# Optimization experiments

Hardware: AMD Instinct MI355X
Metric: run time of the kernel (lower is better)

## Reference

```python
import jax, jax.numpy as jnp
import numpy as np

N_NODES = 51200
N_GRAPHS = 64
NODES_PER_GRAPH = 800
N_EDGES = 819200
DIM_IN = 128
DIM_HIDDEN = 64
HEADS = 3
DIM_OUT = 64


def leaky(x, slope):
    return jnp.where(x >= 0, x, slope * x)


def setup_inputs() -> dict:
    key = jax.random.key(0)
    ks = jax.random.split(key, 12)
    s = lambda fan_in: 1.0 / np.sqrt(fan_in)
    X = jax.random.normal(ks[0], (N_NODES, DIM_IN), dtype=jnp.float32)
    edge_indices = jax.random.randint(ks[1], (2, N_EDGES), 0, N_NODES, dtype=jnp.int32)
    ptr = (jnp.arange(N_GRAPHS + 1, dtype=jnp.int32) * NODES_PER_GRAPH)
    # linearSeq: Linear(dim_in, dim_hidden) + LeakyReLU
    W1 = jax.random.uniform(ks[2], (DIM_IN, DIM_HIDDEN), jnp.float32, -s(DIM_IN), s(DIM_IN))
    b1 = jax.random.uniform(ks[3], (DIM_HIDDEN,), jnp.float32, -s(DIM_IN), s(DIM_IN))
    # GATConv params: lin_src/lin_dst (no bias), att_src/att_dst, bias (concat=False -> out_channels)
    W_src = jax.random.uniform(ks[4], (DIM_HIDDEN, HEADS * DIM_HIDDEN), jnp.float32, -s(DIM_HIDDEN), s(DIM_HIDDEN))
    W_dst = jax.random.uniform(ks[5], (DIM_HIDDEN, HEADS * DIM_HIDDEN), jnp.float32, -s(DIM_HIDDEN), s(DIM_HIDDEN))
    att_src = jax.random.normal(ks[6], (HEADS, DIM_HIDDEN), dtype=jnp.float32) * 0.1
    att_dst = jax.random.normal(ks[7], (HEADS, DIM_HIDDEN), dtype=jnp.float32) * 0.1
    gat_bias = jnp.zeros((DIM_HIDDEN,), dtype=jnp.float32)
    # linear_final: Linear(2*dim_hidden, dim_out)
    Wf = jax.random.uniform(ks[8], (2 * DIM_HIDDEN, DIM_OUT), jnp.float32, -s(2 * DIM_HIDDEN), s(2 * DIM_HIDDEN))
    bf = jax.random.uniform(ks[9], (DIM_OUT,), jnp.float32, -s(2 * DIM_HIDDEN), s(2 * DIM_HIDDEN))
    return {"X": X, "W1": W1, "b1": b1, "W_src": W_src, "W_dst": W_dst,
            "att_src": att_src, "att_dst": att_dst, "gat_bias": gat_bias,
            "Wf": Wf, "bf": bf, "edge_indices": edge_indices, "ptr": ptr}


def reference(X, W1, b1, W_src, W_dst, att_src, att_dst, gat_bias, Wf, bf, edge_indices, ptr):
    N = X.shape[0]
    src, dst = edge_indices[0], edge_indices[1]  # message flows src -> dst
    # input projection
    h = leaky(X @ W1 + b1, 0.01)                                  # [N, DH]
    # GATConv (heads=3, concat=False, add_self_loops=False)
    x_src = (h @ W_src).reshape(N, HEADS, DIM_HIDDEN)             # [N, H, C]
    x_dst = (h @ W_dst).reshape(N, HEADS, DIM_HIDDEN)
    a_src = jnp.einsum('nhc,hc->nh', x_src, att_src)              # [N, H]
    a_dst = jnp.einsum('nhc,hc->nh', x_dst, att_dst)
    logits = leaky(a_src[src] + a_dst[dst], 0.2)                  # [E, H]
    # segment softmax over incoming edges of each target node
    m = jax.ops.segment_max(logits, dst, num_segments=N)          # [N, H]
    e = jnp.exp(logits - m[dst])
    denom = jax.ops.segment_sum(e, dst, num_segments=N)           # [N, H]
    attn = e / denom[dst]                                         # [E, H]
    msg = x_src[src] * attn[..., None]                            # [E, H, C]
    agg = jax.ops.segment_sum(msg, dst, num_segments=N)           # [N, H, C]
    out = agg.mean(axis=1) + gat_bias                             # concat=False -> head mean
    # final head
    cat = jnp.concatenate([h, out], axis=1)                       # [N, 2*DH]
    y = leaky(cat, 0.01) @ Wf + bf                                # [N, DO]
    # aggregate_using_ptr: mean-pool nodes per graph using CSR ptr
    node_graph = jnp.searchsorted(ptr, jnp.arange(N), side='right') - 1
    sums = jax.ops.segment_sum(y, node_graph, num_segments=ptr.shape[0] - 1)
    counts = (ptr[1:] - ptr[:-1]).astype(y.dtype)
    pooled = sums / counts[:, None]                               # [n_graphs, DO]
    return pooled, attn
```

## Files before the change

kernel.cpp:

```cpp
#include <hip/hip_runtime.h>
#include <hip/hip_bf16.h>

#define N_NODES   51200
#define N_GRAPHS  64
#define N_EDGES   819200
#define DIM_IN    128
#define DH        64
#define HEADS     3
#define DIM_OUT   64
#define CAP       96
#define NPART     512
#define PART_SZ   100
#define PBUF_CAP  2048
#define BIN_BLOCKS  400
#define PREP_BLOCKS 116
#define SC_BLOCKS   NPART
#define K1_BLOCKS   (N_NODES / 64)

typedef __hip_bfloat16 bf16;
typedef short bf16x8 __attribute__((ext_vector_type(8)));
typedef float f32x4  __attribute__((ext_vector_type(4)));

__device__ __forceinline__ float b2f(bf16 x) { return __bfloat162float(x); }
__device__ __forceinline__ bf16  f2b(float x) { return __float2bfloat16(x); }
__device__ __forceinline__ short f2bs(float x) { return (short)__bfloat16_as_ushort(f2b(x)); }
__device__ __forceinline__ float leaky(float x, float s) { return x >= 0.f ? x : s * x; }
__device__ __forceinline__ float ldin(const void* p, size_t i, int f32) {
    return f32 ? ((const float*)p)[i] : b2f(((const bf16*)p)[i]);
}
__device__ __forceinline__ bf16x8 ld8(const void* p, size_t i, int f32) {
    if (!f32) return *((const bf16x8*)((const short*)p + i));
    const float* f = (const float*)p + i;
    bf16x8 r;
    #pragma unroll
    for (int j = 0; j < 8; ++j) r[j] = f2bs(f[j]);
    return r;
}

__global__ __launch_bounds__(256) void k_bin_prep(const int* __restrict__ src,
                                                  const int* __restrict__ dst,
                                                  int* __restrict__ pcur,
                                                  unsigned* __restrict__ pbuf,
                                                  const void* __restrict__ X,
                                                  const void* __restrict__ W1,
                                                  const void* __restrict__ Wsrc,
                                                  const void* __restrict__ Wdst,
                                                  const void* __restrict__ Wf,
                                                  const void* __restrict__ att_src,
                                                  const void* __restrict__ att_dst,
                                                  int* __restrict__ flag,
                                                  short* __restrict__ W1t,
                                                  short* __restrict__ Wspt,
                                                  short* __restrict__ Wft,
                                                  short* __restrict__ Wat) {
    const int tid = threadIdx.x;
    if (blockIdx.x < BIN_BLOCKS) {
        __shared__ int cnt[NPART];
        __shared__ int base[NPART];
        cnt[tid] = 0; cnt[tid + 256] = 0;
        __syncthreads();
        const int e0 = blockIdx.x * 2048;
        unsigned pk[8]; int pp[8]; int rr[8];
        #pragma unroll
        for (int t = 0; t < 8; ++t) {
            int e = e0 + t * 256 + tid;
            int s = src[e], d = dst[e];
            int p = d / PART_SZ;
            pk[t] = ((unsigned)s << 16) | (unsigned)(d - p * PART_SZ);
            pp[t] = p;
            rr[t] = atomicAdd(&cnt[p], 1);
        }
        __syncthreads();
        base[tid]       = atomicAdd(&pcur[tid],       cnt[tid]);
        base[tid + 256] = atomicAdd(&pcur[tid + 256], cnt[tid + 256]);
        __syncthreads();
        #pragma unroll
        for (int t = 0; t < 8; ++t) {
            int o = base[pp[t]] + rr[t];
            if (o < PBUF_CAP) pbuf[(size_t)pp[t] * PBUF_CAP + o] = pk[t];
        }
        return;
    }
    if (blockIdx.x < BIN_BLOCKS + PREP_BLOCKS) {
        unsigned ex = (((const unsigned short*)X)[2 * tid] >> 7) & 0xFF;
        int c = __syncthreads_count(ex >= 110 && ex <= 135);
        const int f32 = (c < 128) ? 1 : 0;
        int idx = (blockIdx.x - BIN_BLOCKS) * 256 + tid;
        if (idx < 8192) {
            int n = idx >> 7, k = idx & 127;
            W1t[idx] = f2bs(ldin(W1, (size_t)k * 64 + n, f32));
        } else if (idx < 20480) {
            int j = idx - 8192;
            int col = j / 192;
            int rem = j - col * 192;
            int hh = rem >> 6, kk = rem & 63;
            Wspt[j] = f2bs(ldin(Wsrc, (size_t)kk * 192 + hh * 64 + col, f32) * (1.0f / 3.0f));
        } else if (idx < 28672) {
            int j = idx - 20480;
            int n = j >> 7, k = j & 127;
            Wft[j] = f2bs(ldin(Wf, (size_t)k * 64 + n, f32));
        } else if (idx < 29696) {
            int j = idx - 28672;
            int n = j >> 6, k = j & 63;
            float v = 0.f;
            if (n < 3) {
                for (int c2 = 0; c2 < 64; ++c2)
                    v += ldin(Wsrc, (size_t)k * 192 + n * 64 + c2, f32) * ldin(att_src, n * 64 + c2, f32);
            } else if (n < 6) {
                for (int c2 = 0; c2 < 64; ++c2)
                    v += ldin(Wdst, (size_t)k * 192 + (n - 3) * 64 + c2, f32) * ldin(att_dst, (n - 3) * 64 + c2, f32);
            }
            Wat[j] = f2bs(v);
        }
        return;
    }
    __shared__ int cntp;
    if (tid == 0) cntp = 0;
    __syncthreads();
    int local = 0;
    const unsigned short* Xu = (const unsigned short*)X;
    for (int i = tid * 2; i < 8192; i += 512) {
        unsigned e = (Xu[i] >> 7) & 0xFF;
        if (e >= 110 && e <= 135) local++;
    }
    atomicAdd(&cntp, local);
    __syncthreads();
    if (tid == 0) *flag = (cntp < 2048) ? 1 : 0;
}

__global__ __launch_bounds__(256) void k_scatter_k1(const unsigned* __restrict__ pbuf,
                                                    const int* __restrict__ pcur,
                                                    int* __restrict__ cursor,
                                                    unsigned short* __restrict__ bucket,
                                                    const void* __restrict__ X,
                                                    const short* __restrict__ W1t,
                                                    const short* __restrict__ Wat,
                                                    const void* __restrict__ b1,
                                                    const int* __restrict__ flagp,
                                                    bf16* __restrict__ h_bf,
                                                    unsigned char* __restrict__ h8,
                                                    float* __restrict__ a_src4,
                                                    float* __restrict__ a_dst4) {
    __shared__ short hs[64 * 72];
    __shared__ int cnt2[PART_SZ];
    const int tid = threadIdx.x;
    if (blockIdx.x < SC_BLOCKS) {
        const int p = blockIdx.x;
        const int nbase = p * PART_SZ;
        for (int i = tid; i < PART_SZ; i += 256) cnt2[i] = 0;
        __syncthreads();
        const int pc = min(pcur[p], PBUF_CAP);
        const unsigned* pb = pbuf + (size_t)p * PBUF_CAP;
        for (int i = tid; i < pc; i += 256) {
            unsigned pk = pb[i];
            int dl = (int)(pk & 0xFFFFu);
            int pos = atomicAdd(&cnt2[dl], 1);
            if (pos < CAP) bucket[(size_t)(nbase + dl) * CAP + pos] = (unsigned short)(pk >> 16);
        }
        __syncthreads();
        for (int i = tid; i < PART_SZ; i += 256) cursor[nbase + i] = cnt2[i];
        return;
    }
    const int f32 = *flagp;
    const int w    = tid >> 6;
    const int lane = tid & 63;
    const int lm   = lane & 15;
    const int q    = lane >> 4;
    const int row0 = (blockIdx.x - SC_BLOCKS) * 64;

    const float bias = ldin(b1, w * 16 + lm, f32);
    for (int mt = 0; mt < 4; ++mt) {
        f32x4 acc = {0.f, 0.f, 0.f, 0.f};
        #pragma unroll
        for (int kc = 0; kc < 4; ++kc) {
            bf16x8 a = ld8(X, (size_t)(row0 + mt * 16 + lm) * 128 + kc * 32 + q * 8, f32);
            bf16x8 b = *((const bf16x8*)(W1t + (size_t)(w * 16 + lm) * 128 + kc * 32 + q * 8));
            acc = __builtin_amdgcn_mfma_f32_16x16x32_bf16(a, b, acc, 0, 0, 0);
        }
        #pragma unroll
        for (int r = 0; r < 4; ++r) {
            int row = mt * 16 + q * 4 + r;
            float v = leaky(acc[r] + bias, 0.01f);
            short hv = f2bs(v);
            hs[row * 72 + w * 16 + lm] = hv;
            h_bf[(size_t)(row0 + row) * 64 + w * 16 + lm] = __ushort_as_bfloat16((unsigned short)hv);
            h8[(size_t)(row0 + row) * 64 + w * 16 + lm] =
                (unsigned char)__builtin_amdgcn_cvt_pk_fp8_f32(v, 0.f, 0, false);
        }
    }
    __syncthreads();
    {
        const int mt = w;
        bf16x8 a0  = *((const bf16x8*)(hs + (mt * 16 + lm) * 72 + q * 8));
        bf16x8 a1  = *((const bf16x8*)(hs + (mt * 16 + lm) * 72 + 32 + q * 8));
        bf16x8 b0  = *((const bf16x8*)(Wat + (size_t)lm * 64 + q * 8));
        bf16x8 b1v = *((const bf16x8*)(Wat + (size_t)lm * 64 + 32 + q * 8));
        f32x4 acca = {0.f, 0.f, 0.f, 0.f};
        acca = __builtin_amdgcn_mfma_f32_16x16x32_bf16(a0, b0, acca, 0, 0, 0);
        acca = __builtin_amdgcn_mfma_f32_16x16x32_bf16(a1, b1v, acca, 0, 0, 0);
        if (lm < 6) {
            #pragma unroll
            for (int r = 0; r < 4; ++r) {
                int row = row0 + mt * 16 + q * 4 + r;
                if (lm < 3) a_src4[(size_t)row * 4 + lm] = acca[r];
                else        a_dst4[(size_t)row * 4 + (lm - 3)] = acca[r];
            }
        }
    }
}

__global__ __launch_bounds__(256) void edge_kernel(const unsigned short* __restrict__ bucket,
                                                   const int* __restrict__ cursor,
                                                   const float* __restrict__ a_src4,
                                                   const float* __restrict__ a_dst4,
                                                   const unsigned char* __restrict__ h8,
                                                   float4* __restrict__ dstinfo,
                                                   bf16* __restrict__ wagg) {
    const int lane = threadIdx.x & 63;
    const int w = threadIdx.x >> 6;
    const int n = blockIdx.x * 4 + w;
    const int dg = min(cursor[n], CAP);
    const float4 ad = ((const float4*)a_dst4)[n];
    __shared__ float4 buf[4][64];
    float den0 = 0.f, den1 = 0.f, den2 = 0.f;
    float acc0 = 0.f, acc1 = 0.f, acc2 = 0.f;
    for (int c0 = 0; c0 < dg; c0 += 64) {
        int cnt = min(64, dg - c0);
        if (lane < cnt) {
            int s = bucket[(size_t)n * CAP + c0 + lane];
            const float4 as = ((const float4*)a_src4)[s];
            float e0 = __expf(leaky(as.x + ad.x, 0.2f));
            float e1 = __expf(leaky(as.y + ad.y, 0.2f));
            float e2 = __expf(leaky(as.z + ad.z, 0.2f));
            den0 += e0; den1 += e1; den2 += e2;
            buf[w][lane] = make_float4(e0, e1, e2, __int_as_float(s));
        }
        asm volatile("s_waitcnt lgkmcnt(0)" ::: "memory");
        int j = 0;
        for (; j + 8 <= cnt; j += 8) {
            float4 r[8]; int hv[8];
            #pragma unroll
            for (int u = 0; u < 8; ++u) r[u] = buf[w][j + u];
            #pragma unroll
            for (int u = 0; u < 8; ++u)
                hv[u] = (int)h8[(((unsigned)__float_as_int(r[u].w)) << 6) | (unsigned)lane];
            #pragma unroll
            for (int u = 0; u < 8; ++u) {
                float f = __builtin_amdgcn_cvt_f32_fp8(hv[u], 0);
                acc0 += r[u].x * f; acc1 += r[u].y * f; acc2 += r[u].z * f;
            }
        }
        for (; j < cnt; ++j) {
            float4 r = buf[w][j];
            int hvv = (int)h8[(((unsigned)__float_as_int(r.w)) << 6) | (unsigned)lane];
            float f = __builtin_amdgcn_cvt_f32_fp8(hvv, 0);
            acc0 += r.x * f; acc1 += r.y * f; acc2 += r.z * f;
        }
    }
    #pragma unroll
    for (int off = 32; off >= 1; off >>= 1) {
        den0 += __shfl_xor(den0, off);
        den1 += __shfl_xor(den1, off);
        den2 += __shfl_xor(den2, off);
    }
    float inv0 = den0 > 0.f ? 1.f / den0 : 0.f;
    float inv1 = den1 > 0.f ? 1.f / den1 : 0.f;
    float inv2 = den2 > 0.f ? 1.f / den2 : 0.f;
    size_t wb = (size_t)n * 192;
    wagg[wb + lane]       = f2b(acc0 * inv0);
    wagg[wb + 64 + lane]  = f2b(acc1 * inv1);
    wagg[wb + 128 + lane] = f2b(acc2 * inv2);
    if (lane == 0) {
        dstinfo[(size_t)n * 2 + 0] = make_float4(ad.x, ad.y, ad.z, 0.f);
        dstinfo[(size_t)n * 2 + 1] = make_float4(inv0, inv1, inv2, 0.f);
    }
}

__global__ __launch_bounds__(256) void attn_g3_kernel(const int* __restrict__ src,
                                                      const int* __restrict__ dst,
                                                      const float* __restrict__ a_src4,
                                                      const float4* __restrict__ dstinfo,
                                                      const bf16* __restrict__ h_bf,
                                                      const bf16* __restrict__ wagg,
                                                      const short* __restrict__ Wspt,
                                                      const short* __restrict__ Wft,
                                                      const void* __restrict__ gat_bias,
                                                      const void* __restrict__ bfv,
                                                      const int* __restrict__ flagp,
                                                      const int* __restrict__ gptr,
                                                      float* __restrict__ psum,
                                                      int* __restrict__ done,
                                                      void* __restrict__ d_out) {
    const int f32 = *flagp;
    __shared__ short cs[64 * 136];
    __shared__ int sptr[N_GRAPHS + 1];
    __shared__ int rowg_s[64];
    __shared__ int readyg[64];
    __shared__ int nready;
    if (blockIdx.x < N_EDGES / 256) {
        int e = blockIdx.x * 256 + threadIdx.x;
        int s = src[e], d = dst[e];
        const float4 as = ((const float4*)a_src4)[s];
        const float4 ad = dstinfo[(size_t)d * 2 + 0];
        const float4 cv = dstinfo[(size_t)d * 2 + 1];
        float a0 = __expf(leaky(as.x + ad.x, 0.2f)) * cv.x;
        float a1 = __expf(leaky(as.y + ad.y, 0.2f)) * cv.y;
        float a2 = __expf(leaky(as.z + ad.z, 0.2f)) * cv.z;
        size_t o = (size_t)N_GRAPHS * DIM_OUT + (size_t)e * 3;
        if (f32) {
            float* p = (float*)d_out;
            p[o] = a0; p[o + 1] = a1; p[o + 2] = a2;
        } else {
            bf16* p = (bf16*)d_out;
            p[o] = f2b(a0); p[o + 1] = f2b(a1); p[o + 2] = f2b(a2);
        }
        return;
    }
    const int bid  = blockIdx.x - N_EDGES / 256;
    const int tid  = threadIdx.x;
    const int w    = tid >> 6;
    const int lane = tid & 63;
    const int lm   = lane & 15;
    const int q    = lane >> 4;
    const int row0 = bid * 64;
    if (tid <= N_GRAPHS) sptr[tid] = gptr[tid];
    if (tid == 0) nready = 0;
    __syncthreads();
    if (tid < 64) {
        int row = row0 + tid;
        int lo2 = 0, hi2 = N_GRAPHS;
        while (hi2 - lo2 > 1) { int mid = (lo2 + hi2) >> 1; if (sptr[mid] <= row) lo2 = mid; else hi2 = mid; }
        rowg_s[tid] = lo2;
    }
    for (int idx = tid; idx < 64 * 64; idx += 256) {
        int r = idx >> 6, k = idx & 63;
        cs[r * 136 + k] = f2bs(leaky(b2f(h_bf[(size_t)(row0 + r) * 64 + k]), 0.01f));
    }
    {
        const int col = w * 16 + lm;
        const float gb = ldin(gat_bias, col, f32);
        for (int mt = 0; mt < 4; ++mt) {
            f32x4 acc = {0.f, 0.f, 0.f, 0.f};
            #pragma unroll
            for (int kc = 0; kc < 6; ++kc) {
                bf16x8 a = *((const bf16x8*)((const short*)wagg + (size_t)(row0 + mt * 16 + lm) * 192 + kc * 32 + q * 8));
                bf16x8 b = *((const bf16x8*)(Wspt + (size_t)col * 192 + kc * 32 + q * 8));
                acc = __builtin_amdgcn_mfma_f32_16x16x32_bf16(a, b, acc, 0, 0, 0);
            }
            #pragma unroll
            for (int r = 0; r < 4; ++r) {
                int row = mt * 16 + q * 4 + r;
                cs[row * 136 + 64 + col] = f2bs(leaky(acc[r] + gb, 0.01f));
            }
        }
    }
    __syncthreads();
    {
        const int col = w * 16 + lm;
        const float bias = ldin(bfv, col, f32);
        int curg = -1; float runsum = 0.f;
        for (int mt = 0; mt < 4; ++mt) {
            f32x4 acc = {0.f, 0.f, 0.f, 0.f};
            #pragma unroll
            for (int kc = 0; kc < 4; ++kc) {
                bf16x8 a = *((const bf16x8*)(cs + (mt * 16 + lm) * 136 + kc * 32 + q * 8));
                bf16x8 b = *((const bf16x8*)(Wft + (size_t)col * 128 + kc * 32 + q * 8));
                acc = __builtin_amdgcn_mfma_f32_16x16x32_bf16(a, b, acc, 0, 0, 0);
            }
            #pragma unroll
            for (int r = 0; r < 4; ++r) {
                int lrow = mt * 16 + q * 4 + r;
                float v = acc[r] + bias;
                int g = rowg_s[lrow];
                if (g != curg) {
                    if (curg >= 0) atomicAdd(&psum[curg * 64 + col], runsum);
                    curg = g; runsum = 0.f;
                }
                runsum += v;
            }
        }
        if (curg >= 0) atomicAdd(&psum[curg * 64 + col], runsum);
    }
    __syncthreads();
    if (tid == 0) {
        int g0 = rowg_s[0], g1 = rowg_s[63];
        int nr = 0;
        for (int g = g0; g <= g1; ++g) {
            int lo = sptr[g], hi = sptr[g + 1];
            if (hi <= lo) continue;
            int expected = (hi - 1) / 64 - lo / 64 + 1;
            int old = atomicAdd(&done[g], 1);
            if (old == expected - 1) readyg[nr++] = g;
        }
        nready = nr;
    }
    __syncthreads();
    for (int i = 0; i < nready; ++i) {
        int g = readyg[i];
        if (tid < 64) {
            float s = atomicAdd(&psum[g * 64 + tid], 0.0f);
            float v = s / (float)(sptr[g + 1] - sptr[g]);
            if (f32) ((float*)d_out)[g * DIM_OUT + tid] = v;
            else     ((bf16*)d_out)[g * DIM_OUT + tid]  = f2b(v);
        }
    }
}

extern "C" void kernel_launch(void* const* d_in, const int* in_sizes, int n_in,
                              void* d_out, int out_size, void* d_ws, size_t ws_size,
                              hipStream_t stream) {
    const void* X        = d_in[0];
    const void* W1       = d_in[1];
    const void* b1       = d_in[2];
    const void* Wsrc     = d_in[3];
    const void* Wdst     = d_in[4];
    const void* att_src  = d_in[5];
    const void* att_dst  = d_in[6];
    const void* gat_bias = d_in[7];
    const void* Wf       = d_in[8];
    const void* bfv      = d_in[9];
    const int*  ei       = (const int*)d_in[10];
    const int*  ptr      = (const int*)d_in[11];
    const int*  src  = ei;
    const int*  dstp = ei + N_EDGES;

    char* ws = (char*)d_ws;
    size_t off_b = 0;
    auto alloc = [&](size_t bytes) -> char* {
        char* p = ws + off_b;
        off_b += (bytes + 255) & ~(size_t)255;
        return p;
    };
    int*     flag    = (int*)    alloc(256);
    short*   W1t     = (short*)  alloc(8192 * 2);
    short*   Wspt    = (short*)  alloc(12288 * 2);
    short*   Wft     = (short*)  alloc(8192 * 2);
    short*   Wat     = (short*)  alloc(1024 * 2);
    bf16*    h_bf    = (bf16*)   alloc((size_t)N_NODES * 64 * 2);
    unsigned char* h8 = (unsigned char*)alloc((size_t)N_NODES * 64);
    float*   a_src4  = (float*)  alloc((size_t)N_NODES * 16);
    float*   a_dst4  = (float*)  alloc((size_t)N_NODES * 16);
    float4*  dstinfo = (float4*) alloc((size_t)N_NODES * 2 * 16);
    bf16*    wagg    = (bf16*)   alloc((size_t)N_NODES * 192 * 2);
    float*   psum    = (float*)  alloc((size_t)N_GRAPHS * 64 * 4);
    int*     done    = (int*)    alloc(256);
    int*     pcur    = (int*)    alloc(NPART * 4);
    int*     cursor  = (int*)    alloc((size_t)N_NODES * 4);
    unsigned short* bucket = (unsigned short*)alloc((size_t)N_NODES * CAP * 2);
    unsigned* pbuf   = (unsigned*)wagg;
    if (off_b > ws_size) return;

    hipMemsetAsync(psum, 0, (size_t)N_GRAPHS * 64 * 4 + 256 + NPART * 4, stream);
    hipLaunchKernelGGL(k_bin_prep, dim3(BIN_BLOCKS + PREP_BLOCKS + 1), dim3(256), 0, stream,
                       src, dstp, pcur, pbuf,
                       X, W1, Wsrc, Wdst, Wf, att_src, att_dst, flag, W1t, Wspt, Wft, Wat);
    hipLaunchKernelGGL(k_scatter_k1, dim3(SC_BLOCKS + K1_BLOCKS), dim3(256), 0, stream,
                       pbuf, pcur, cursor, bucket,
                       X, W1t, Wat, b1, flag, h_bf, h8, a_src4, a_dst4);
    hipLaunchKernelGGL(edge_kernel, dim3(N_NODES / 4), dim3(256), 0, stream,
                       bucket, cursor, a_src4, a_dst4, h8, dstinfo, wagg);
    hipLaunchKernelGGL(attn_g3_kernel, dim3(N_EDGES / 256 + N_NODES / 64), dim3(256), 0, stream,
                       src, dstp, a_src4, dstinfo, h_bf, wagg, Wspt, Wft,
                       gat_bias, bfv, flag, ptr, psum, done, d_out);
}
```

Baseline: 205.1 us.

## Move node projection into first kernel with per-block weight prep in LDS

The X@W1 projection and attention-logit GEMM move from the second kernel into the first fused kernel. Each of those blocks now builds the transposed W1 and the fused attention weights in shared memory itself, so neither is precomputed into global memory. That leaves the second kernel as a pure bucket scatter and lets the GEMM overlap with edge binning. The cost is redundant weight transposition, including a 64-term dot product per attention weight, repeated in each of 800 blocks, plus a larger LDS footprint per block.

```diff
diff --git a/kernel.cpp b/kernel.cpp
--- a/kernel.cpp
+++ b/kernel.cpp
@@ -12,10 +12,10 @@
 #define NPART     512
 #define PART_SZ   100
 #define PBUF_CAP  2048
-#define BIN_BLOCKS  400
-#define PREP_BLOCKS 116
-#define SC_BLOCKS   NPART
 #define K1_BLOCKS   (N_NODES / 64)
+#define BIN_BLOCKS  (N_EDGES / 2048)
+#define PREP_BLOCKS 80
+#define A_BLOCKS    (K1_BLOCKS + BIN_BLOCKS + PREP_BLOCKS + 1)
 
 typedef __hip_bfloat16 bf16;
 typedef short bf16x8 __attribute__((ext_vector_type(8)));
@@ -37,29 +37,103 @@
     return r;
 }
 
-__global__ __launch_bounds__(256) void k_bin_prep(const int* __restrict__ src,
-                                                  const int* __restrict__ dst,
-                                                  int* __restrict__ pcur,
-                                                  unsigned* __restrict__ pbuf,
-                                                  const void* __restrict__ X,
-                                                  const void* __restrict__ W1,
-                                                  const void* __restrict__ Wsrc,
-                                                  const void* __restrict__ Wdst,
-                                                  const void* __restrict__ Wf,
-                                                  const void* __restrict__ att_src,
-                                                  const void* __restrict__ att_dst,
-                                                  int* __restrict__ flag,
-                                                  short* __restrict__ W1t,
-                                                  short* __restrict__ Wspt,
-                                                  short* __restrict__ Wft,
-                                                  short* __restrict__ Wat) {
+__global__ __launch_bounds__(256) void k_fused_a(const int* __restrict__ src,
+                                                 const int* __restrict__ dst,
+                                                 int* __restrict__ pcur,
+                                                 unsigned* __restrict__ pbuf,
+                                                 const void* __restrict__ X,
+                                                 const void* __restrict__ W1,
+                                                 const void* __restrict__ Wsrc,
+                                                 const void* __restrict__ Wdst,
+                                                 const void* __restrict__ Wf,
+                                                 const void* __restrict__ att_src,
+                                                 const void* __restrict__ att_dst,
+                                                 const void* __restrict__ b1,
+                                                 int* __restrict__ flag,
+                                                 short* __restrict__ Wspt,
+                                                 short* __restrict__ Wft,
+                                                 bf16* __restrict__ h_bf,
+                                                 unsigned char* __restrict__ h8,
+                                                 float* __restrict__ a_src4,
+                                                 float* __restrict__ a_dst4) {
+    __shared__ __align__(16) char smem[28672];
     const int tid = threadIdx.x;
-    if (blockIdx.x < BIN_BLOCKS) {
-        __shared__ int cnt[NPART];
-        __shared__ int base[NPART];
+    if (blockIdx.x < K1_BLOCKS) {
+        unsigned ex = (((const unsigned short*)X)[2 * tid] >> 7) & 0xFF;
+        int cpr = __syncthreads_count(ex >= 110 && ex <= 135);
+        const int f32 = (cpr < 128) ? 1 : 0;
+        short* w1t = (short*)smem;
+        short* wat = (short*)(smem + 17408);
+        short* hs  = (short*)(smem + 19456);
+        for (int idx = tid; idx < 8192; idx += 256) {
+            int n = idx >> 7, k = idx & 127;
+            w1t[n * 136 + k] = f2bs(ldin(W1, (size_t)k * 64 + n, f32));
+        }
+        for (int j = tid; j < 1024; j += 256) {
+            int n = j >> 6, k = j & 63;
+            float v = 0.f;
+            if (n < 3) {
+                for (int c2 = 0; c2 < 64; ++c2)
+                    v += ldin(Wsrc, (size_t)k * 192 + n * 64 + c2, f32) * ldin(att_src, n * 64 + c2, f32);
+            } else if (n < 6) {
+                for (int c2 = 0; c2 < 64; ++c2)
+                    v += ldin(Wdst, (size_t)k * 192 + (n - 3) * 64 + c2, f32) * ldin(att_dst, (n - 3) * 64 + c2, f32);
+            }
+            wat[j] = f2bs(v);
+        }
+        __syncthreads();
+        const int w    = tid >> 6;
+        const int lane = tid & 63;
+        const int lm   = lane & 15;
+        const int q    = lane >> 4;
+        const int row0 = blockIdx.x * 64;
+        const float bias = ldin(b1, w * 16 + lm, f32);
+        for (int mt = 0; mt < 4; ++mt) {
+            f32x4 acc = {0.f, 0.f, 0.f, 0.f};
+            #pragma unroll
+            for (int kc = 0; kc < 4; ++kc) {
+                bf16x8 a = ld8(X, (size_t)(row0 + mt * 16 + lm) * 128 + kc * 32 + q * 8, f32);
+                bf16x8 b = *((const bf16x8*)(w1t + (w * 16 + lm) * 136 + kc * 32 + q * 8));
+                acc = __builtin_amdgcn_mfma_f32_16x16x32_bf16(a, b, acc, 0, 0, 0);
+            }
+            #pragma unroll
+            for (int r = 0; r < 4; ++r) {
+                int row = mt * 16 + q * 4 + r;
+                float v = leaky(acc[r] + bias, 0.01f);
+                short hv = f2bs(v);
+                hs[row * 72 + w * 16 + lm] = hv;
+                h_bf[(size_t)(row0 + row) * 64 + w * 16 + lm] = __ushort_as_bfloat16((unsigned short)hv);
+                h8[(size_t)(row0 + row) * 64 + w * 16 + lm] =
+                    (unsigned char)__builtin_amdgcn_cvt_pk_fp8_f32(v, 0.f, 0, false);
+            }
+        }
+        __syncthreads();
+        {
+            const int mt = w;
+            bf16x8 a0  = *((const bf16x8*)(hs + (mt * 16 + lm) * 72 + q * 8));
+            bf16x8 a1  = *((const bf16x8*)(hs + (mt * 16 + lm) * 72 + 32 + q * 8));
+            bf16x8 b0  = *((const bf16x8*)(wat + (size_t)lm * 64 + q * 8));
+            bf16x8 b1v = *((const bf16x8*)(wat + (size_t)lm * 64 + 32 + q * 8));
+            f32x4 acca = {0.f, 0.f, 0.f, 0.f};
+            acca = __builtin_amdgcn_mfma_f32_16x16x32_bf16(a0, b0, acca, 0, 0, 0);
+            acca = __builtin_amdgcn_mfma_f32_16x16x32_bf16(a1, b1v, acca, 0, 0, 0);
+            if (lm < 6) {
+                #pragma unroll
+                for (int r = 0; r < 4; ++r) {
+                    int row = row0 + mt * 16 + q * 4 + r;
+                    if (lm < 3) a_src4[(size_t)row * 4 + lm] = acca[r];
+                    else        a_dst4[(size_t)row * 4 + (lm - 3)] = acca[r];
+                }
+            }
+        }
+        return;
+    }
+    if (blockIdx.x < K1_BLOCKS + BIN_BLOCKS) {
+        int* cnt  = (int*)smem;
+        int* base = cnt + NPART;
         cnt[tid] = 0; cnt[tid + 256] = 0;
         __syncthreads();
-        const int e0 = blockIdx.x * 2048;
+        const int e0 = (blockIdx.x - K1_BLOCKS) * 2048;
         unsigned pk[8]; int pp[8]; int rr[8];
         #pragma unroll
         for (int t = 0; t < 8; ++t) {
@@ -81,41 +155,25 @@
         }
         return;
     }
-    if (blockIdx.x < BIN_BLOCKS + PREP_BLOCKS) {
+    if (blockIdx.x < K1_BLOCKS + BIN_BLOCKS + PREP_BLOCKS) {
         unsigned ex = (((const unsigned short*)X)[2 * tid] >> 7) & 0xFF;
         int c = __syncthreads_count(ex >= 110 && ex <= 135);
         const int f32 = (c < 128) ? 1 : 0;
-        int idx = (blockIdx.x - BIN_BLOCKS) * 256 + tid;
-        if (idx < 8192) {
-            int n = idx >> 7, k = idx & 127;
-            W1t[idx] = f2bs(ldin(W1, (size_t)k * 64 + n, f32));
-        } else if (idx < 20480) {
-            int j = idx - 8192;
-            int col = j / 192;
-            int rem = j - col * 192;
+        int idx = (blockIdx.x - K1_BLOCKS - BIN_BLOCKS) * 256 + tid;
+        if (idx < 12288) {
+            int col = idx / 192;
+            int rem = idx - col * 192;
             int hh = rem >> 6, kk = rem & 63;
-            Wspt[j] = f2bs(ldin(Wsrc, (size_t)kk * 192 + hh * 64 + col, f32) * (1.0f / 3.0f));
-        } else if (idx < 28672) {
-            int j = idx - 20480;
+            Wspt[idx] = f2bs(ldin(Wsrc, (size_t)kk * 192 + hh * 64 + col, f32) * (1.0f / 3.0f));
+        } else {
+            int j = idx - 12288;
             int n = j >> 7, k = j & 127;
             Wft[j] = f2bs(ldin(Wf, (size_t)k * 64 + n, f32));
-        } else if (idx < 29696) {
-            int j = idx - 28672;
-            int n = j >> 6, k = j & 63;
-            float v = 0.f;
-            if (n < 3) {
-                for (int c2 = 0; c2 < 64; ++c2)
-                    v += ldin(Wsrc, (size_t)k * 192 + n * 64 + c2, f32) * ldin(att_src, n * 64 + c2, f32);
-            } else if (n < 6) {
-                for (int c2 = 0; c2 < 64; ++c2)
-                    v += ldin(Wdst, (size_t)k * 192 + (n - 3) * 64 + c2, f32) * ldin(att_dst, (n - 3) * 64 + c2, f32);
-            }
-            Wat[j] = f2bs(v);
         }
         return;
     }
-    __shared__ int cntp;
-    if (tid == 0) cntp = 0;
+    int* cntp = (int*)smem;
+    if (tid == 0) *cntp = 0;
     __syncthreads();
     int local = 0;
     const unsigned short* Xu = (const unsigned short*)X;
@@ -123,90 +181,31 @@
         unsigned e = (Xu[i] >> 7) & 0xFF;
         if (e >= 110 && e <= 135) local++;
     }
-    atomicAdd(&cntp, local);
-    __syncthreads();
-    if (tid == 0) *flag = (cntp < 2048) ? 1 : 0;
-}
-
-__global__ __launch_bounds__(256) void k_scatter_k1(const unsigned* __restrict__ pbuf,
-                                                    const int* __restrict__ pcur,
-                                                    int* __restrict__ cursor,
-                                                    unsigned short* __restrict__ bucket,
-                                                    const void* __restrict__ X,
-                                                    const short* __restrict__ W1t,
-                                                    const short* __restrict__ Wat,
-                                                    const void* __restrict__ b1,
-                                                    const int* __restrict__ flagp,
-                                                    bf16* __restrict__ h_bf,
-                                                    unsigned char* __restrict__ h8,
-                                                    float* __restrict__ a_src4,
-                                                    float* __restrict__ a_dst4) {
-    __shared__ short hs[64 * 72];
+    atomicAdd(cntp, local);
+    __syncthreads();
+    if (tid == 0) *flag = (*cntp < 2048) ? 1 : 0;
+}
+
+__global__ __launch_bounds__(256) void k_scatter(const unsigned* __restrict__ pbuf,
+                                                 const int* __restrict__ pcur,
+                                                 int* __restrict__ cursor,
+                                                 unsigned short* __restrict__ bucket) {
     __shared__ int cnt2[PART_SZ];
     const int tid = threadIdx.x;
-    if (blockIdx.x < SC_BLOCKS) {
-        const int p = blockIdx.x;
-        const int nbase = p * PART_SZ;
-        for (int i = tid; i < PART_SZ; i += 256) cnt2[i] = 0;
-        __syncthreads();
-        const int pc = min(pcur[p], PBUF_CAP);
-        const unsigned* pb = pbuf + (size_t)p * PBUF_CAP;
-        for (int i = tid; i < pc; i += 256) {
-            unsigned pk = pb[i];
-            int dl = (int)(pk & 0xFFFFu);
-            int pos = atomicAdd(&cnt2[dl], 1);
-            if (pos < CAP) bucket[(size_t)(nbase + dl) * CAP + pos] = (unsigned short)(pk >> 16);
-        }
-        __syncthreads();
-        for (int i = tid; i < PART_SZ; i += 256) cursor[nbase + i] = cnt2[i];
-        return;
-    }
-    const int f32 = *flagp;
-    const int w    = tid >> 6;
-    const int lane = tid & 63;
-    const int lm   = lane & 15;
-    const int q    = lane >> 4;
-    const int row0 = (blockIdx.x - SC_BLOCKS) * 64;
-
-    const float bias = ldin(b1, w * 16 + lm, f32);
-    for (int mt = 0; mt < 4; ++mt) {
-        f32x4 acc = {0.f, 0.f, 0.f, 0.f};
-        #pragma unroll
-        for (int kc = 0; kc < 4; ++kc) {
-            bf16x8 a = ld8(X, (size_t)(row0 + mt * 16 + lm) * 128 + kc * 32 + q * 8, f32);
-            bf16x8 b = *((const bf16x8*)(W1t + (size_t)(w * 16 + lm) * 128 + kc * 32 + q * 8));
-            acc = __builtin_amdgcn_mfma_f32_16x16x32_bf16(a, b, acc, 0, 0, 0);
-        }
-        #pragma unroll
-        for (int r = 0; r < 4; ++r) {
-            int row = mt * 16 + q * 4 + r;
-            float v = leaky(acc[r] + bias, 0.01f);
-            short hv = f2bs(v);
-            hs[row * 72 + w * 16 + lm] = hv;
-            h_bf[(size_t)(row0 + row) * 64 + w * 16 + lm] = __ushort_as_bfloat16((unsigned short)hv);
-            h8[(size_t)(row0 + row) * 64 + w * 16 + lm] =
-                (unsigned char)__builtin_amdgcn_cvt_pk_fp8_f32(v, 0.f, 0, false);
-        }
-    }
-    __syncthreads();
-    {
-        const int mt = w;
-        bf16x8 a0  = *((const bf16x8*)(hs + (mt * 16 + lm) * 72 + q * 8));
-        bf16x8 a1  = *((const bf16x8*)(hs + (mt * 16 + lm) * 72 + 32 + q * 8));
-        bf16x8 b0  = *((const bf16x8*)(Wat + (size_t)lm * 64 + q * 8));
-        bf16x8 b1v = *((const bf16x8*)(Wat + (size_t)lm * 64 + 32 + q * 8));
-        f32x4 acca = {0.f, 0.f, 0.f, 0.f};
-        acca = __builtin_amdgcn_mfma_f32_16x16x32_bf16(a0, b0, acca, 0, 0, 0);
-        acca = __builtin_amdgcn_mfma_f32_16x16x32_bf16(a1, b1v, acca, 0, 0, 0);
-        if (lm < 6) {
-            #pragma unroll
-            for (int r = 0; r < 4; ++r) {
-                int row = row0 + mt * 16 + q * 4 + r;
-                if (lm < 3) a_src4[(size_t)row * 4 + lm] = acca[r];
-                else        a_dst4[(size_t)row * 4 + (lm - 3)] = acca[r];
-            }
-        }
-    }
+    const int p = blockIdx.x;
+    const int nbase = p * PART_SZ;
+    for (int i = tid; i < PART_SZ; i += 256) cnt2[i] = 0;
+    __syncthreads();
+    const int pc = min(pcur[p], PBUF_CAP);
+    const unsigned* pb = pbuf + (size_t)p * PBUF_CAP;
+    for (int i = tid; i < pc; i += 256) {
+        unsigned pk = pb[i];
+        int dl = (int)(pk & 0xFFFFu);
+        int pos = atomicAdd(&cnt2[dl], 1);
+        if (pos < CAP) bucket[(size_t)(nbase + dl) * CAP + pos] = (unsigned short)(pk >> 16);
+    }
+    __syncthreads();
+    for (int i = tid; i < PART_SZ; i += 256) cursor[nbase + i] = cnt2[i];
 }
 
 __global__ __launch_bounds__(256) void edge_kernel(const unsigned short* __restrict__ bucket,
@@ -432,10 +431,8 @@
         return p;
     };
     int*     flag    = (int*)    alloc(256);
-    short*   W1t     = (short*)  alloc(8192 * 2);
     short*   Wspt    = (short*)  alloc(12288 * 2);
     short*   Wft     = (short*)  alloc(8192 * 2);
-    short*   Wat     = (short*)  alloc(1024 * 2);
     bf16*    h_bf    = (bf16*)   alloc((size_t)N_NODES * 64 * 2);
     unsigned char* h8 = (unsigned char*)alloc((size_t)N_NODES * 64);
     float*   a_src4  = (float*)  alloc((size_t)N_NODES * 16);
@@ -451,12 +448,12 @@
     if (off_b > ws_size) return;
 
     hipMemsetAsync(psum, 0, (size_t)N_GRAPHS * 64 * 4 + 256 + NPART * 4, stream);
-    hipLaunchKernelGGL(k_bin_prep, dim3(BIN_BLOCKS + PREP_BLOCKS + 1), dim3(256), 0, stream,
+    hipLaunchKernelGGL(k_fused_a, dim3(A_BLOCKS), dim3(256), 0, stream,
                        src, dstp, pcur, pbuf,
-                       X, W1, Wsrc, Wdst, Wf, att_src, att_dst, flag, W1t, Wspt, Wft, Wat);
-    hipLaunchKernelGGL(k_scatter_k1, dim3(SC_BLOCKS + K1_BLOCKS), dim3(256), 0, stream,
-                       pbuf, pcur, cursor, bucket,
-                       X, W1t, Wat, b1, flag, h_bf, h8, a_src4, a_dst4);
+                       X, W1, Wsrc, Wdst, Wf, att_src, att_dst, b1,
+                       flag, Wspt, Wft, h_bf, h8, a_src4, a_dst4);
+    hipLaunchKernelGGL(k_scatter, dim3(NPART), dim3(256), 0, stream,
+                       pbuf, pcur, cursor, bucket);
     hipLaunchKernelGGL(edge_kernel, dim3(N_NODES / 4), dim3(256), 0, stream,
                        bucket, cursor, a_src4, a_dst4, h8, dstinfo, wagg);
     hipLaunchKernelGGL(attn_g3_kernel, dim3(N_EDGES / 256 + N_NODES / 64), dim3(256), 0, stream,
```

Result: slower. 263.7 us (+28.5%).
